# Performance work log

Measured on AMD Instinct MI355X. Metric: run time of the kernel, lower is better.

Reference implementation:

```python
import jax, jax.numpy as jnp
import numpy as np

TEMPERATURE = 10.0
N_CLASSES = 10


def _sqdist(a, b):
    # squared euclidean distances, [Na, Nb] == torch.cdist(a, b) ** 2
    an = jnp.sum(a * a, axis=1)[:, None]
    bn = jnp.sum(b * b, axis=1)[None, :]
    return jnp.maximum(an + bn - 2.0 * (a @ b.T), 0.0)


def setup_inputs() -> dict:
    key = jax.random.key(0)
    ks = jax.random.split(key, 6)
    B, N, D, H, C = 512, 4096, 512, 2048, N_CLASSES
    return {
        "x": jax.random.normal(ks[0], (B, D), dtype=jnp.float32),
        "star_features": jax.random.normal(ks[1], (N, D), dtype=jnp.float32),
        "from_features": jax.random.normal(ks[2], (N, D), dtype=jnp.float32),
        "star_label_ids": jax.random.randint(ks[3], (N,), 0, C),
        "W1": jax.random.normal(ks[4], (D, H), dtype=jnp.float32) * 0.02,
        "b1": jnp.zeros((H,), dtype=jnp.float32),
        "W2": jax.random.normal(ks[5], (H, C), dtype=jnp.float32) * 0.02,
        "b2": jnp.zeros((C,), dtype=jnp.float32),
    }


def _transport_features(x, feats_to, star_feats):
    # dists: [N_star, B]
    d = _sqdist(star_feats, x)
    d = d / jnp.mean(d, axis=0, keepdims=True)
    e = jnp.exp(-TEMPERATURE * d)                    # [N_star, B]
    w = feats_to.T @ e                               # [d_to, B]
    return (w / jnp.sum(e, axis=0, keepdims=True)).T  # [B, d_to]


def reference(x, star_features, from_features, star_label_ids, W1, b1, W2, b2):
    B = x.shape[0]
    C = N_CLASSES
    # --- exact-match lookup against dataset_star features (fused eq+all reduce) ---
    mask = jnp.all(x[:, None, :] == star_features[None, :, :], axis=2)  # [B, N_star]
    matched = jnp.any(mask, axis=1)                                      # [B]
    match_idx = jnp.argmax(mask, axis=1)                                 # [B]
    # --- transport features: matched samples take aligned dataset sample, rest use OT map ---
    xt_unmatched = _transport_features(x, from_features, star_features)  # [B, d]
    xt_matched = from_features[match_idx]                                # [B, d]
    x_transported = jnp.where(matched[:, None], xt_matched, xt_unmatched)
    # --- run the model in the transported domain (MLP classifier) ---
    h = jax.nn.relu(x_transported @ W1 + b1)
    logits = h @ W2 + b2                                                 # [B, C]
    # --- project_labels: preds and one-hot unique labels have equal dim -> cdist/argmin branch ---
    unique_labels = jnp.eye(C, dtype=logits.dtype)
    closest = jnp.argmin(_sqdist(logits, unique_labels), axis=1)
    y_proj = unique_labels[closest]                                      # [B, C] (unused by 'all_features')
    # --- transport_labels, method='all_features': feature-distance-weighted average of star labels ---
    d2 = _sqdist(from_features, x_transported)                           # [N_from, B]
    d2 = d2 / jnp.mean(d2, axis=0, keepdims=True)
    e2 = jnp.exp(-TEMPERATURE * d2)
    star_labels = jax.nn.one_hot(star_label_ids, C, dtype=x.dtype)       # [N_star, C]
    y_star = (star_labels.T @ e2 / jnp.sum(e2, axis=0, keepdims=True)).T  # [B, C]
    # single (model, dataset) pair -> sum/len is identity
    return y_star
```

## Files before the change

### kernel.cpp

```cpp
#include <hip/hip_runtime.h>

#define TEMP 10.0f
#define NS 4096
#define BB 512
#define DDIM 512
#define NCLS 10
#define LDSP 72

typedef short bf16x8 __attribute__((ext_vector_type(8)));
typedef float f32x4 __attribute__((ext_vector_type(4)));

__device__ inline short f2bf(float f) {
    unsigned u = __builtin_bit_cast(unsigned, f);
    u += 0x7FFFu + ((u >> 16) & 1u);
    return (short)(u >> 16);
}
__device__ inline float bf2f(short h) {
    unsigned u = ((unsigned)(unsigned short)h) << 16;
    return __builtin_bit_cast(float, u);
}

__global__ __launch_bounds__(256)
void prep(const float* __restrict__ x, const float* __restrict__ star,
          const float* __restrict__ from,
          short* __restrict__ Xb, short* __restrict__ Sb,
          short* __restrict__ FTb, short* __restrict__ Fb,
          float* __restrict__ xn2, float* __restrict__ sn2, float* __restrict__ fn2,
          float* __restrict__ scol, float* __restrict__ xcol, int* __restrict__ midx)
{
    int bid = blockIdx.x, t = threadIdx.x;
    if (bid < 2176) {
        const float* in; short* outb; float* n2; float* colb; int rowbase;
        if (bid < 1024)      { in = star; outb = Sb; n2 = sn2; colb = scol; rowbase = bid * 4; }
        else if (bid < 1152) { in = x;    outb = Xb; n2 = xn2; colb = xcol; rowbase = (bid - 1024) * 4; }
        else                 { in = from; outb = Fb; n2 = fn2; colb = nullptr; rowbase = (bid - 1152) * 4; }
        if (bid == 1024) { midx[t] = NS; midx[256 + t] = NS; }
        int row = rowbase + (t >> 6);
        int l = t & 63;
        const float4* p = (const float4*)(in + (size_t)row * DDIM) + l * 2;
        float4 a = p[0], b = p[1];
        float s = a.x*a.x + a.y*a.y + a.z*a.z + a.w*a.w
                + b.x*b.x + b.y*b.y + b.z*b.z + b.w*b.w;
        bf16x8 h;
        h[0]=f2bf(a.x); h[1]=f2bf(a.y); h[2]=f2bf(a.z); h[3]=f2bf(a.w);
        h[4]=f2bf(b.x); h[5]=f2bf(b.y); h[6]=f2bf(b.z); h[7]=f2bf(b.w);
        *(bf16x8*)(outb + (size_t)row * DDIM + l * 8) = h;
        #pragma unroll
        for (int off = 32; off > 0; off >>= 1) s += __shfl_down(s, off);
        if (l == 0) {
            n2[row] = s;
            if (colb) colb[row] = a.x;
        }
        return;
    }
    __shared__ short tile[64][LDSP];
    int tid2 = bid - 2176;
    int n0 = (tid2 & 63) * 64, d0 = (tid2 >> 6) * 64;
    int r = t >> 4, c4 = (t & 15) * 4;
    #pragma unroll
    for (int rr = 0; rr < 64; rr += 16) {
        float4 v = *(const float4*)(from + (size_t)(n0 + r + rr) * DDIM + d0 + c4);
        tile[r + rr][c4 + 0] = f2bf(v.x);
        tile[r + rr][c4 + 1] = f2bf(v.y);
        tile[r + rr][c4 + 2] = f2bf(v.z);
        tile[r + rr][c4 + 3] = f2bf(v.w);
    }
    __syncthreads();
    int dr = t >> 2, nco = (t & 3) * 16;
    short tmp[16];
    #pragma unroll
    for (int q = 0; q < 16; ++q) tmp[q] = tile[nco + q][dr];
    short* op = FTb + (size_t)(d0 + dr) * NS + n0 + nco;
    *(bf16x8*)op       = *(bf16x8*)tmp;
    *(bf16x8*)(op + 8) = *(bf16x8*)(tmp + 8);
}

__global__ __launch_bounds__(256)
void match16(const float* __restrict__ x, const float* __restrict__ star,
             const float* __restrict__ scol, const float* __restrict__ xcol,
             int* __restrict__ midx)
{
    __shared__ float xl[BB];
    int t = threadIdx.x;
    *(float2*)&xl[t * 2] = *(const float2*)&xcol[t * 2];
    __syncthreads();
    int n = blockIdx.x * 256 + t;
    float sv = scol[n];
    #pragma unroll 4
    for (int b4 = 0; b4 < BB; b4 += 4) {
        float4 xv = *(const float4*)&xl[b4];
        if (xv.x == sv || xv.y == sv || xv.z == sv || xv.w == sv) {
            #pragma unroll
            for (int j = 0; j < 4; ++j) {
                int b = b4 + j;
                if (xl[b] == sv) {
                    const float* xr = x + (size_t)b * DDIM;
                    const float* sr = star + (size_t)n * DDIM;
                    bool eq = true;
                    for (int k = 0; k < DDIM && eq; k += 4) {
                        float4 a = *(const float4*)(xr + k);
                        float4 c = *(const float4*)(sr + k);
                        eq = (a.x == c.x) && (a.y == c.y) &&
                             (a.z == c.z) && (a.w == c.w);
                    }
                    if (eq) atomicMin(&midx[b], n);
                }
            }
        }
    }
}

__global__ __launch_bounds__(256)
void gemm_bt(const short* __restrict__ A, const short* __restrict__ B, int K,
             int kslab, int nt, float* __restrict__ C, int ldc, size_t cstride)
{
    __shared__ short As[2][64][LDSP];
    __shared__ short Bs[2][128][LDSP];
    int t = threadIdx.x;
    int m0 = blockIdx.x * 64;
    int n0 = blockIdx.y * 128;
    int kbase = blockIdx.z * kslab;
    float* Cp = C + (size_t)blockIdx.z * cstride;
    int wid = t >> 6, lane = t & 63;
    int wr = wid >> 1, wc = wid & 1;
    int lr = lane & 15, lk = lane >> 4;

    int ar = t >> 2, ak = (t & 3) * 16;
    int br = t >> 1, bk = (t & 1) * 32;
    const short* Ag = A + (size_t)(m0 + ar) * K + kbase + ak;
    const short* Bg = B + (size_t)(n0 + br) * K + kbase + bk;

    f32x4 acc[2][4] = {};
    bf16x8 ra0 = *(const bf16x8*)Ag;
    bf16x8 ra1 = *(const bf16x8*)(Ag + 8);
    bf16x8 rb0 = *(const bf16x8*)Bg;
    bf16x8 rb1 = *(const bf16x8*)(Bg + 8);
    bf16x8 rb2 = *(const bf16x8*)(Bg + 16);
    bf16x8 rb3 = *(const bf16x8*)(Bg + 24);
    int cur = 0;
    *(bf16x8*)&As[0][ar][ak]      = ra0;
    *(bf16x8*)&As[0][ar][ak + 8]  = ra1;
    *(bf16x8*)&Bs[0][br][bk]      = rb0;
    *(bf16x8*)&Bs[0][br][bk + 8]  = rb1;
    *(bf16x8*)&Bs[0][br][bk + 16] = rb2;
    *(bf16x8*)&Bs[0][br][bk + 24] = rb3;

    for (int it = 0; it < nt; ++it) {
        __syncthreads();
        if (it + 1 < nt) {
            int ko = (it + 1) * 64;
            ra0 = *(const bf16x8*)(Ag + ko);
            ra1 = *(const bf16x8*)(Ag + ko + 8);
            rb0 = *(const bf16x8*)(Bg + ko);
            rb1 = *(const bf16x8*)(Bg + ko + 8);
            rb2 = *(const bf16x8*)(Bg + ko + 16);
            rb3 = *(const bf16x8*)(Bg + ko + 24);
        }
        #pragma unroll
        for (int ks = 0; ks < 2; ++ks) {
            int k0 = ks * 32 + lk * 8;
            bf16x8 af[2], bfr[4];
            #pragma unroll
            for (int i = 0; i < 2; ++i)
                af[i] = *(const bf16x8*)&As[cur][wr * 32 + i * 16 + lr][k0];
            #pragma unroll
            for (int j = 0; j < 4; ++j)
                bfr[j] = *(const bf16x8*)&Bs[cur][wc * 64 + j * 16 + lr][k0];
            #pragma unroll
            for (int i = 0; i < 2; ++i)
                #pragma unroll
                for (int j = 0; j < 4; ++j)
                    acc[i][j] = __builtin_amdgcn_mfma_f32_16x16x32_bf16(
                        af[i], bfr[j], acc[i][j], 0, 0, 0);
        }
        if (it + 1 < nt) {
            cur ^= 1;
            *(bf16x8*)&As[cur][ar][ak]      = ra0;
            *(bf16x8*)&As[cur][ar][ak + 8]  = ra1;
            *(bf16x8*)&Bs[cur][br][bk]      = rb0;
            *(bf16x8*)&Bs[cur][br][bk + 8]  = rb1;
            *(bf16x8*)&Bs[cur][br][bk + 16] = rb2;
            *(bf16x8*)&Bs[cur][br][bk + 24] = rb3;
        }
    }
    #pragma unroll
    for (int i = 0; i < 2; ++i) {
        #pragma unroll
        for (int r = 0; r < 4; ++r) {
            int gm = m0 + wr * 32 + i * 16 + lk * 4 + r;
            #pragma unroll
            for (int j = 0; j < 4; ++j) {
                int gn = n0 + wc * 64 + j * 16 + lr;
                Cp[(size_t)gm * ldc + gn] = acc[i][j][r];
            }
        }
    }
}

__device__ inline float block_sum(float s, float* red) {
    #pragma unroll
    for (int off = 32; off > 0; off >>= 1) s += __shfl_down(s, off);
    int wid = threadIdx.x >> 6;
    if ((threadIdx.x & 63) == 0) red[wid] = s;
    __syncthreads();
    float tot = red[0] + red[1] + red[2] + red[3];
    __syncthreads();
    return tot;
}

__global__ __launch_bounds__(256)
void exp_sq(const float* __restrict__ dTp, const float* __restrict__ an2,
            const float* __restrict__ bn2, short* __restrict__ eT,
            float* __restrict__ sumE)
{
    __shared__ float red[4];
    int b = blockIdx.x;
    int t = threadIdx.x;
    const float* p0 = dTp + (size_t)b * NS;
    const float* p1 = p0 + (size_t)BB * NS;
    float a2 = an2[b];
    float v[16];
    float s = 0.f;
    #pragma unroll
    for (int q = 0; q < 4; ++q) {
        int n = t * 16 + q * 4;
        float4 u0 = *(const float4*)(p0 + n);
        float4 u1 = *(const float4*)(p1 + n);
        float4 n2 = *(const float4*)(bn2 + n);
        float4 w;
        w.x = fmaxf(a2 + n2.x - 2.0f * (u0.x + u1.x), 0.f);
        w.y = fmaxf(a2 + n2.y - 2.0f * (u0.y + u1.y), 0.f);
        w.z = fmaxf(a2 + n2.z - 2.0f * (u0.z + u1.z), 0.f);
        w.w = fmaxf(a2 + n2.w - 2.0f * (u0.w + u1.w), 0.f);
        v[q*4+0] = w.x; v[q*4+1] = w.y; v[q*4+2] = w.z; v[q*4+3] = w.w;
        s += w.x + w.y + w.z + w.w;
    }
    float tot = block_sum(s, red);
    float scale = -TEMP * (float)NS / tot;
    float se = 0.f;
    bf16x8 h0, h1;
    #pragma unroll
    for (int e = 0; e < 16; ++e) {
        float ev = __expf(v[e] * scale);
        short hh = f2bf(ev);
        se += bf2f(hh);
        if (e < 8) h0[e] = hh; else h1[e - 8] = hh;
    }
    short* op = eT + (size_t)b * NS + t * 16;
    *(bf16x8*)op       = h0;
    *(bf16x8*)(op + 8) = h1;
    float setot = block_sum(se, red);
    if (t == 0) sumE[b] = setot;
}

__global__ __launch_bounds__(256)
void xt_fin(const float* __restrict__ wpart, const float* __restrict__ sumE,
            const int* __restrict__ midx, const float* __restrict__ fromf,
            short* __restrict__ xtb, float* __restrict__ xtn2)
{
    __shared__ float red[4];
    int b = blockIdx.x;
    int t = threadIdx.x;
    int d = t * 2;
    int mi = midx[b];
    float inv = 1.0f / sumE[b];
    float v0 = 0.f, v1 = 0.f;
    #pragma unroll
    for (int sl = 0; sl < 16; ++sl) {
        float2 p = *(const float2*)(wpart + (size_t)sl * (BB * DDIM) + (size_t)b * DDIM + d);
        v0 += p.x; v1 += p.y;
    }
    v0 *= inv; v1 *= inv;
    if (mi < NS) {
        v0 = fromf[(size_t)mi * DDIM + d];
        v1 = fromf[(size_t)mi * DDIM + d + 1];
    }
    xtb[(size_t)b * DDIM + d]     = f2bf(v0);
    xtb[(size_t)b * DDIM + d + 1] = f2bf(v1);
    float tot = block_sum(v0 * v0 + v1 * v1, red);
    if (t == 0) xtn2[b] = tot;
}

__global__ __launch_bounds__(256)
void ystar_sq(const float* __restrict__ d2p, const float* __restrict__ an2,
              const float* __restrict__ bn2, const int* __restrict__ labels,
              float* __restrict__ out)
{
    __shared__ float red[4];
    __shared__ float cred[NCLS + 1][4];
    int b = blockIdx.x;
    int t = threadIdx.x;
    const float* p0 = d2p + (size_t)b * NS;
    const float* p1 = p0 + (size_t)BB * NS;
    float a2 = an2[b];
    float v[16];
    float s = 0.f;
    #pragma unroll
    for (int q = 0; q < 4; ++q) {
        int n = t * 16 + q * 4;
        float4 u0 = *(const float4*)(p0 + n);
        float4 u1 = *(const float4*)(p1 + n);
        float4 n2 = *(const float4*)(bn2 + n);
        float4 w;
        w.x = fmaxf(a2 + n2.x - 2.0f * (u0.x + u1.x), 0.f);
        w.y = fmaxf(a2 + n2.y - 2.0f * (u0.y + u1.y), 0.f);
        w.z = fmaxf(a2 + n2.z - 2.0f * (u0.z + u1.z), 0.f);
        w.w = fmaxf(a2 + n2.w - 2.0f * (u0.w + u1.w), 0.f);
        v[q*4+0] = w.x; v[q*4+1] = w.y; v[q*4+2] = w.z; v[q*4+3] = w.w;
        s += w.x + w.y + w.z + w.w;
    }
    float tot = block_sum(s, red);
    float scale = -TEMP * (float)NS / tot;
    float accs[NCLS] = {};
    float te = 0.f;
    #pragma unroll
    for (int q = 0; q < 4; ++q) {
        int4 lb = *(const int4*)(labels + t * 16 + q * 4);
        int lbl[4] = {lb.x, lb.y, lb.z, lb.w};
        #pragma unroll
        for (int e = 0; e < 4; ++e) {
            float ev = __expf(v[q * 4 + e] * scale);
            te += ev;
            #pragma unroll
            for (int c = 0; c < NCLS; ++c) accs[c] += (lbl[e] == c) ? ev : 0.f;
        }
    }
    int wid = t >> 6, lane = t & 63;
    #pragma unroll
    for (int c = 0; c < NCLS + 1; ++c) {
        float sv = (c < NCLS) ? accs[c] : te;
        #pragma unroll
        for (int off = 32; off > 0; off >>= 1) sv += __shfl_down(sv, off);
        if (lane == 0) cred[c][wid] = sv;
    }
    __syncthreads();
    if (t < NCLS) {
        float num = cred[t][0] + cred[t][1] + cred[t][2] + cred[t][3];
        float den = cred[NCLS][0] + cred[NCLS][1] + cred[NCLS][2] + cred[NCLS][3];
        out[b * NCLS + t] = num / den;
    }
}

extern "C" void kernel_launch(void* const* d_in, const int* in_sizes, int n_in,
                              void* d_out, int out_size, void* d_ws, size_t ws_size,
                              hipStream_t stream) {
    const float* x     = (const float*)d_in[0];
    const float* star  = (const float*)d_in[1];
    const float* from  = (const float*)d_in[2];
    const int*   label = (const int*)d_in[3];
    float* out = (float*)d_out;

    float* F = (float*)d_ws;
    float* dTp   = F;
    float* wpart = F + 4194304;
    float* d2p   = F + 8388608;
    short* Sb    = (short*)(F + 12582912);
    short* FTb   = (short*)(F + 13631488);
    short* Fb    = (short*)(F + 14680064);
    short* Eb    = (short*)(F + 15728640);
    short* Xb    = (short*)(F + 16777216);
    short* XTb   = (short*)(F + 16908288);
    float* sn2   = F + 17039360;
    float* fn2   = F + 17043456;
    float* xn2   = F + 17047552;
    float* xtn2  = F + 17048064;
    float* sumE  = F + 17048576;
    float* scol  = F + 17049088;
    float* xcol  = F + 17053184;
    int*   midx  = (int*)(F + 17053696);

    prep<<<2688, 256, 0, stream>>>(x, star, from, Xb, Sb, FTb, Fb,
                                   xn2, sn2, fn2, scol, xcol, midx);
    match16<<<16, 256, 0, stream>>>(x, star, scol, xcol, midx);
    gemm_bt<<<dim3(8, 32, 2), 256, 0, stream>>>(Xb, Sb, DDIM, 256, 4, dTp, NS,
                                                (size_t)BB * NS);
    exp_sq<<<BB, 256, 0, stream>>>(dTp, xn2, sn2, Eb, sumE);
    gemm_bt<<<dim3(8, 4, 16), 256, 0, stream>>>(Eb, FTb, NS, 256, 4, wpart, DDIM,
                                                (size_t)BB * DDIM);
    xt_fin<<<BB, 256, 0, stream>>>(wpart, sumE, midx, from, XTb, xtn2);
    gemm_bt<<<dim3(8, 32, 2), 256, 0, stream>>>(XTb, Fb, DDIM, 256, 4, d2p, NS,
                                                (size_t)BB * NS);
    ystar_sq<<<BB, 256, 0, stream>>>(d2p, xtn2, fn2, label, out);
}
```

Measured before the change: 76.03 us.

## Compute distance means analytically and fuse exp epilogue into distance GEMMs

```diff
diff --git a/kernel.cpp b/kernel.cpp
--- a/kernel.cpp
+++ b/kernel.cpp
@@ -18,6 +18,46 @@
 __device__ inline float bf2f(short h) {
     unsigned u = ((unsigned)(unsigned short)h) << 16;
     return __builtin_bit_cast(float, u);
+}
+
+__device__ inline float block_sum(float s, float* red) {
+    #pragma unroll
+    for (int off = 32; off > 0; off >>= 1) s += __shfl_down(s, off);
+    int wid = threadIdx.x >> 6;
+    if ((threadIdx.x & 63) == 0) red[wid] = s;
+    __syncthreads();
+    float tot = red[0] + red[1] + red[2] + red[3];
+    __syncthreads();
+    return tot;
+}
+
+__global__ __launch_bounds__(256)
+void colmeans(const float* __restrict__ star, const float* __restrict__ from,
+              float* __restrict__ sbar, float* __restrict__ fbar,
+              float* __restrict__ sssp, float* __restrict__ fssp)
+{
+    __shared__ float csl[8][33];
+    __shared__ float red[4];
+    int bid = blockIdx.x, t = threadIdx.x;
+    const float* M; float* outm; float* outss; int ib;
+    if (bid < 16) { M = star; outm = sbar; outss = sssp; ib = bid; }
+    else          { M = from; outm = fbar; outss = fssp; ib = bid - 16; }
+    int d0 = ib * 32, rg = t >> 5, dc = t & 31;
+    float cs = 0.f, sq = 0.f;
+    #pragma unroll 4
+    for (int r = rg; r < NS; r += 8) {
+        float v = M[(size_t)r * DDIM + d0 + dc];
+        cs += v; sq += v * v;
+    }
+    csl[rg][dc] = cs;
+    float sqt = block_sum(sq, red);
+    if (t == 0) outss[ib] = sqt;
+    if (t < 32) {
+        float s = 0.f;
+        #pragma unroll
+        for (int q = 0; q < 8; ++q) s += csl[q][t];
+        outm[d0 + t] = s * (1.0f / NS);
+    }
 }
 
 __global__ __launch_bounds__(256)
@@ -76,6 +116,29 @@
 }
 
 __global__ __launch_bounds__(256)
+void scale1(const float* __restrict__ x, const float* __restrict__ sbar,
+            const float* __restrict__ sssp, const float* __restrict__ xn2,
+            float* __restrict__ escale1)
+{
+    int t = threadIdx.x;
+    int lane = t & 63, w = t >> 6;
+    int b = blockIdx.x * 4 + w;
+    const float4* xp = (const float4*)(x + (size_t)b * DDIM) + lane * 2;
+    const float4* sp = (const float4*)sbar + lane * 2;
+    float4 xa = xp[0], xb = xp[1], sa = sp[0], sb = sp[1];
+    float dot = xa.x*sa.x + xa.y*sa.y + xa.z*sa.z + xa.w*sa.w
+              + xb.x*sb.x + xb.y*sb.y + xb.z*sb.z + xb.w*sb.w;
+    float ss = (lane < 16) ? sssp[lane] : 0.f;
+    #pragma unroll
+    for (int m = 32; m > 0; m >>= 1) {
+        dot += __shfl_xor(dot, m);
+        ss  += __shfl_xor(ss, m);
+    }
+    if (lane == 0)
+        escale1[b] = -TEMP / (ss * (1.0f / NS) + xn2[b] - 2.0f * dot);
+}
+
+__global__ __launch_bounds__(256)
 void match16(const float* __restrict__ x, const float* __restrict__ star,
              const float* __restrict__ scol, const float* __restrict__ xcol,
              int* __restrict__ midx)
@@ -110,25 +173,28 @@
     }
 }
 
-__global__ __launch_bounds__(256)
-void gemm_bt(const short* __restrict__ A, const short* __restrict__ B, int K,
-             int kslab, int nt, float* __restrict__ C, int ldc, size_t cstride)
+template<int WSE>
+__global__ __launch_bounds__(256)
+void gemm_exp(const short* __restrict__ A, const short* __restrict__ B,
+              const float* __restrict__ an2, const float* __restrict__ bn2,
+              const float* __restrict__ escale, short* __restrict__ Eout,
+              float* __restrict__ sumEp)
 {
     __shared__ short As[2][64][LDSP];
     __shared__ short Bs[2][128][LDSP];
+    __shared__ float se[2][64];
+    const int K = DDIM;
     int t = threadIdx.x;
     int m0 = blockIdx.x * 64;
     int n0 = blockIdx.y * 128;
-    int kbase = blockIdx.z * kslab;
-    float* Cp = C + (size_t)blockIdx.z * cstride;
     int wid = t >> 6, lane = t & 63;
     int wr = wid >> 1, wc = wid & 1;
     int lr = lane & 15, lk = lane >> 4;
 
     int ar = t >> 2, ak = (t & 3) * 16;
     int br = t >> 1, bk = (t & 1) * 32;
-    const short* Ag = A + (size_t)(m0 + ar) * K + kbase + ak;
-    const short* Bg = B + (size_t)(n0 + br) * K + kbase + bk;
+    const short* Ag = A + (size_t)(m0 + ar) * K + ak;
+    const short* Bg = B + (size_t)(n0 + br) * K + bk;
 
     f32x4 acc[2][4] = {};
     bf16x8 ra0 = *(const bf16x8*)Ag;
@@ -145,6 +211,7 @@
     *(bf16x8*)&Bs[0][br][bk + 16] = rb2;
     *(bf16x8*)&Bs[0][br][bk + 24] = rb3;
 
+    const int nt = K / 64;
     for (int it = 0; it < nt; ++it) {
         __syncthreads();
         if (it + 1 < nt) {
@@ -183,6 +250,111 @@
             *(bf16x8*)&Bs[cur][br][bk + 24] = rb3;
         }
     }
+    float bn2v[4];
+    int gnv[4];
+    #pragma unroll
+    for (int j = 0; j < 4; ++j) { gnv[j] = n0 + wc * 64 + j * 16 + lr; bn2v[j] = bn2[gnv[j]]; }
+    #pragma unroll
+    for (int i = 0; i < 2; ++i) {
+        #pragma unroll
+        for (int r = 0; r < 4; ++r) {
+            int gm = m0 + wr * 32 + i * 16 + lk * 4 + r;
+            float a2 = an2[gm];
+            float sc = escale[gm];
+            float rs = 0.f;
+            #pragma unroll
+            for (int j = 0; j < 4; ++j) {
+                float dv = fmaxf(a2 + bn2v[j] - 2.0f * acc[i][j][r], 0.0f);
+                short hb = f2bf(__expf(dv * sc));
+                Eout[(size_t)gm * NS + gnv[j]] = hb;
+                if (WSE) rs += bf2f(hb);
+            }
+            if (WSE) {
+                #pragma unroll
+                for (int m = 1; m < 16; m <<= 1) rs += __shfl_xor(rs, m);
+                if (lr == 0) se[wc][wr * 32 + i * 16 + lk * 4 + r] = rs;
+            }
+        }
+    }
+    if (WSE) {
+        __syncthreads();
+        if (t < 64) sumEp[(size_t)(m0 + t) * 32 + blockIdx.y] = se[0][t] + se[1][t];
+    }
+}
+
+__global__ __launch_bounds__(256)
+void gemm_bt(const short* __restrict__ A, const short* __restrict__ B, int K,
+             int kslab, int nt, float* __restrict__ C, int ldc, size_t cstride)
+{
+    __shared__ short As[2][64][LDSP];
+    __shared__ short Bs[2][128][LDSP];
+    int t = threadIdx.x;
+    int m0 = blockIdx.x * 64;
+    int n0 = blockIdx.y * 128;
+    int kbase = blockIdx.z * kslab;
+    float* Cp = C + (size_t)blockIdx.z * cstride;
+    int wid = t >> 6, lane = t & 63;
+    int wr = wid >> 1, wc = wid & 1;
+    int lr = lane & 15, lk = lane >> 4;
+
+    int ar = t >> 2, ak = (t & 3) * 16;
+    int br = t >> 1, bk = (t & 1) * 32;
+    const short* Ag = A + (size_t)(m0 + ar) * K + kbase + ak;
+    const short* Bg = B + (size_t)(n0 + br) * K + kbase + bk;
+
+    f32x4 acc[2][4] = {};
+    bf16x8 ra0 = *(const bf16x8*)Ag;
+    bf16x8 ra1 = *(const bf16x8*)(Ag + 8);
+    bf16x8 rb0 = *(const bf16x8*)Bg;
+    bf16x8 rb1 = *(const bf16x8*)(Bg + 8);
+    bf16x8 rb2 = *(const bf16x8*)(Bg + 16);
+    bf16x8 rb3 = *(const bf16x8*)(Bg + 24);
+    int cur = 0;
+    *(bf16x8*)&As[0][ar][ak]      = ra0;
+    *(bf16x8*)&As[0][ar][ak + 8]  = ra1;
+    *(bf16x8*)&Bs[0][br][bk]      = rb0;
+    *(bf16x8*)&Bs[0][br][bk + 8]  = rb1;
+    *(bf16x8*)&Bs[0][br][bk + 16] = rb2;
+    *(bf16x8*)&Bs[0][br][bk + 24] = rb3;
+
+    for (int it = 0; it < nt; ++it) {
+        __syncthreads();
+        if (it + 1 < nt) {
+            int ko = (it + 1) * 64;
+            ra0 = *(const bf16x8*)(Ag + ko);
+            ra1 = *(const bf16x8*)(Ag + ko + 8);
+            rb0 = *(const bf16x8*)(Bg + ko);
+            rb1 = *(const bf16x8*)(Bg + ko + 8);
+            rb2 = *(const bf16x8*)(Bg + ko + 16);
+            rb3 = *(const bf16x8*)(Bg + ko + 24);
+        }
+        #pragma unroll
+        for (int ks = 0; ks < 2; ++ks) {
+            int k0 = ks * 32 + lk * 8;
+            bf16x8 af[2], bfr[4];
+            #pragma unroll
+            for (int i = 0; i < 2; ++i)
+                af[i] = *(const bf16x8*)&As[cur][wr * 32 + i * 16 + lr][k0];
+            #pragma unroll
+            for (int j = 0; j < 4; ++j)
+                bfr[j] = *(const bf16x8*)&Bs[cur][wc * 64 + j * 16 + lr][k0];
+            #pragma unroll
+            for (int i = 0; i < 2; ++i)
+                #pragma unroll
+                for (int j = 0; j < 4; ++j)
+                    acc[i][j] = __builtin_amdgcn_mfma_f32_16x16x32_bf16(
+                        af[i], bfr[j], acc[i][j], 0, 0, 0);
+        }
+        if (it + 1 < nt) {
+            cur ^= 1;
+            *(bf16x8*)&As[cur][ar][ak]      = ra0;
+            *(bf16x8*)&As[cur][ar][ak + 8]  = ra1;
+            *(bf16x8*)&Bs[cur][br][bk]      = rb0;
+            *(bf16x8*)&Bs[cur][br][bk + 8]  = rb1;
+            *(bf16x8*)&Bs[cur][br][bk + 16] = rb2;
+            *(bf16x8*)&Bs[cur][br][bk + 24] = rb3;
+        }
+    }
     #pragma unroll
     for (int i = 0; i < 2; ++i) {
         #pragma unroll
@@ -197,79 +369,37 @@
     }
 }
 
-__device__ inline float block_sum(float s, float* red) {
-    #pragma unroll
-    for (int off = 32; off > 0; off >>= 1) s += __shfl_down(s, off);
-    int wid = threadIdx.x >> 6;
-    if ((threadIdx.x & 63) == 0) red[wid] = s;
-    __syncthreads();
-    float tot = red[0] + red[1] + red[2] + red[3];
-    __syncthreads();
-    return tot;
-}
-
-__global__ __launch_bounds__(256)
-void exp_sq(const float* __restrict__ dTp, const float* __restrict__ an2,
-            const float* __restrict__ bn2, short* __restrict__ eT,
-            float* __restrict__ sumE)
+__global__ __launch_bounds__(256)
+void xt_fin(const float* __restrict__ wpart, const float* __restrict__ sumEp,
+            const int* __restrict__ midx, const float* __restrict__ fromf,
+            const float* __restrict__ fbar, const float* __restrict__ fssp,
+            short* __restrict__ xtb, float* __restrict__ xtn2,
+            float* __restrict__ escale2)
 {
     __shared__ float red[4];
-    int b = blockIdx.x;
-    int t = threadIdx.x;
-    const float* p0 = dTp + (size_t)b * NS;
-    const float* p1 = p0 + (size_t)BB * NS;
-    float a2 = an2[b];
-    float v[16];
-    float s = 0.f;
-    #pragma unroll
-    for (int q = 0; q < 4; ++q) {
-        int n = t * 16 + q * 4;
-        float4 u0 = *(const float4*)(p0 + n);
-        float4 u1 = *(const float4*)(p1 + n);
-        float4 n2 = *(const float4*)(bn2 + n);
-        float4 w;
-        w.x = fmaxf(a2 + n2.x - 2.0f * (u0.x + u1.x), 0.f);
-        w.y = fmaxf(a2 + n2.y - 2.0f * (u0.y + u1.y), 0.f);
-        w.z = fmaxf(a2 + n2.z - 2.0f * (u0.z + u1.z), 0.f);
-        w.w = fmaxf(a2 + n2.w - 2.0f * (u0.w + u1.w), 0.f);
-        v[q*4+0] = w.x; v[q*4+1] = w.y; v[q*4+2] = w.z; v[q*4+3] = w.w;
-        s += w.x + w.y + w.z + w.w;
-    }
-    float tot = block_sum(s, red);
-    float scale = -TEMP * (float)NS / tot;
-    float se = 0.f;
-    bf16x8 h0, h1;
-    #pragma unroll
-    for (int e = 0; e < 16; ++e) {
-        float ev = __expf(v[e] * scale);
-        short hh = f2bf(ev);
-        se += bf2f(hh);
-        if (e < 8) h0[e] = hh; else h1[e - 8] = hh;
-    }
-    short* op = eT + (size_t)b * NS + t * 16;
-    *(bf16x8*)op       = h0;
-    *(bf16x8*)(op + 8) = h1;
-    float setot = block_sum(se, red);
-    if (t == 0) sumE[b] = setot;
-}
-
-__global__ __launch_bounds__(256)
-void xt_fin(const float* __restrict__ wpart, const float* __restrict__ sumE,
-            const int* __restrict__ midx, const float* __restrict__ fromf,
-            short* __restrict__ xtb, float* __restrict__ xtn2)
-{
-    __shared__ float red[4];
+    __shared__ float bc[2];
     int b = blockIdx.x;
     int t = threadIdx.x;
     int d = t * 2;
     int mi = midx[b];
-    float inv = 1.0f / sumE[b];
+    if (t == 0) {
+        float s = 0.f;
+        #pragma unroll
+        for (int k = 0; k < 32; ++k) s += sumEp[(size_t)b * 32 + k];
+        float f = 0.f;
+        #pragma unroll
+        for (int k = 0; k < 16; ++k) f += fssp[k];
+        bc[0] = 1.0f / s;
+        bc[1] = f * (1.0f / NS);
+    }
     float v0 = 0.f, v1 = 0.f;
     #pragma unroll
     for (int sl = 0; sl < 16; ++sl) {
         float2 p = *(const float2*)(wpart + (size_t)sl * (BB * DDIM) + (size_t)b * DDIM + d);
         v0 += p.x; v1 += p.y;
     }
+    __syncthreads();
+    float inv = bc[0], fmean = bc[1];
     v0 *= inv; v1 *= inv;
     if (mi < NS) {
         v0 = fromf[(size_t)mi * DDIM + d];
@@ -277,40 +407,25 @@
     }
     xtb[(size_t)b * DDIM + d]     = f2bf(v0);
     xtb[(size_t)b * DDIM + d + 1] = f2bf(v1);
-    float tot = block_sum(v0 * v0 + v1 * v1, red);
-    if (t == 0) xtn2[b] = tot;
-}
-
-__global__ __launch_bounds__(256)
-void ystar_sq(const float* __restrict__ d2p, const float* __restrict__ an2,
-              const float* __restrict__ bn2, const int* __restrict__ labels,
-              float* __restrict__ out)
-{
-    __shared__ float red[4];
+    float nt2 = block_sum(v0 * v0 + v1 * v1, red);
+    float2 fb2 = *(const float2*)(fbar + d);
+    float fd = block_sum(v0 * fb2.x + v1 * fb2.y, red);
+    if (t == 0) {
+        xtn2[b] = nt2;
+        escale2[b] = -TEMP / (fmean + nt2 - 2.0f * fd);
+    }
+}
+
+__global__ __launch_bounds__(256)
+void ystar_fin(const short* __restrict__ e2T, const int* __restrict__ labels,
+               float* __restrict__ out)
+{
     __shared__ float cred[NCLS + 1][4];
     int b = blockIdx.x;
     int t = threadIdx.x;
-    const float* p0 = d2p + (size_t)b * NS;
-    const float* p1 = p0 + (size_t)BB * NS;
-    float a2 = an2[b];
-    float v[16];
-    float s = 0.f;
-    #pragma unroll
-    for (int q = 0; q < 4; ++q) {
-        int n = t * 16 + q * 4;
-        float4 u0 = *(const float4*)(p0 + n);
-        float4 u1 = *(const float4*)(p1 + n);
-        float4 n2 = *(const float4*)(bn2 + n);
-        float4 w;
-        w.x = fmaxf(a2 + n2.x - 2.0f * (u0.x + u1.x), 0.f);
-        w.y = fmaxf(a2 + n2.y - 2.0f * (u0.y + u1.y), 0.f);
-        w.z = fmaxf(a2 + n2.z - 2.0f * (u0.z + u1.z), 0.f);
-        w.w = fmaxf(a2 + n2.w - 2.0f * (u0.w + u1.w), 0.f);
-        v[q*4+0] = w.x; v[q*4+1] = w.y; v[q*4+2] = w.z; v[q*4+3] = w.w;
-        s += w.x + w.y + w.z + w.w;
-    }
-    float tot = block_sum(s, red);
-    float scale = -TEMP * (float)NS / tot;
+    const short* row = e2T + (size_t)b * NS + t * 16;
+    bf16x8 h0 = *(const bf16x8*)row;
+    bf16x8 h1 = *(const bf16x8*)(row + 8);
     float accs[NCLS] = {};
     float te = 0.f;
     #pragma unroll
@@ -319,7 +434,8 @@
         int lbl[4] = {lb.x, lb.y, lb.z, lb.w};
         #pragma unroll
         for (int e = 0; e < 4; ++e) {
-            float ev = __expf(v[q * 4 + e] * scale);
+            int idx = q * 4 + e;
+            float ev = bf2f(idx < 8 ? h0[idx] : h1[idx - 8]);
             te += ev;
             #pragma unroll
             for (int c = 0; c < NCLS; ++c) accs[c] += (lbl[e] == c) ? ev : 0.f;
@@ -351,34 +467,39 @@
     float* out = (float*)d_out;
 
     float* F = (float*)d_ws;
-    float* dTp   = F;
-    float* wpart = F + 4194304;
-    float* d2p   = F + 8388608;
-    short* Sb    = (short*)(F + 12582912);
-    short* FTb   = (short*)(F + 13631488);
-    short* Fb    = (short*)(F + 14680064);
-    short* Eb    = (short*)(F + 15728640);
-    short* Xb    = (short*)(F + 16777216);
-    short* XTb   = (short*)(F + 16908288);
-    float* sn2   = F + 17039360;
-    float* fn2   = F + 17043456;
-    float* xn2   = F + 17047552;
-    float* xtn2  = F + 17048064;
-    float* sumE  = F + 17048576;
-    float* scol  = F + 17049088;
-    float* xcol  = F + 17053184;
-    int*   midx  = (int*)(F + 17053696);
-
+    float* wpart = F;
+    short* Sb    = (short*)(F + 4194304);
+    short* FTb   = (short*)(F + 5242880);
+    short* Fb    = (short*)(F + 6291456);
+    short* Eb    = (short*)(F + 7340032);
+    short* E2b   = (short*)(F + 8388608);
+    short* Xb    = (short*)(F + 9437184);
+    short* XTb   = (short*)(F + 9568256);
+    float* sn2   = F + 9699328;
+    float* fn2   = F + 9703424;
+    float* xn2   = F + 9707520;
+    float* xtn2  = F + 9708032;
+    float* esc1  = F + 9708544;
+    float* esc2  = F + 9709056;
+    float* sbar  = F + 9709568;
+    float* fbar  = F + 9710080;
+    float* sssp  = F + 9710592;
+    float* fssp  = F + 9710608;
+    float* sumEp = F + 9710624;
+    float* scol  = F + 9727008;
+    float* xcol  = F + 9731104;
+    int*   midx  = (int*)(F + 9731616);
+
+    colmeans<<<32, 256, 0, stream>>>(star, from, sbar, fbar, sssp, fssp);
     prep<<<2688, 256, 0, stream>>>(x, star, from, Xb, Sb, FTb, Fb,
                                    xn2, sn2, fn2, scol, xcol, midx);
+    scale1<<<128, 256, 0, stream>>>(x, sbar, sssp, xn2, esc1);
     match16<<<16, 256, 0, stream>>>(x, star, scol, xcol, midx);
-    gemm_bt<<<dim3(8, 32, 2), 256, 0, stream>>>(Xb, Sb, DDIM, 256, 4, dTp, NS,
-                                                (size_t)BB * NS);
-    exp_sq<<<BB, 256, 0, stream>>>(dTp, xn2, sn2, Eb, sumE);
+    gemm_exp<1><<<dim3(8, 32), 256, 0, stream>>>(Xb, Sb, xn2, sn2, esc1, Eb, sumEp);
     gemm_bt<<<dim3(8, 4, 16), 256, 0, stream>>>(Eb, FTb, NS, 256, 4, wpart, DDIM,
                                                 (size_t)BB * DDIM);
-    xt_fin<<<BB, 256, 0, stream>>>(wpart, sumE, midx, from, XTb, xtn2);
-    gemm_bt<<<dim3(8, 32, 2), 256, 0, stream>>>(XTb, Fb, DDIM, 256, 4, d2p, NS,
-                                                (size_t)BB * NS);
-    ystar_sq<<<BB, 256, 0, stream>>>(d2p, xtn2, fn2, label, out);
-}
+    xt_fin<<<BB, 256, 0, stream>>>(wpart, sumEp, midx, from, fbar, fssp,
+                                   XTb, xtn2, esc2);
+    gemm_exp<0><<<dim3(8, 32), 256, 0, stream>>>(XTb, Fb, xtn2, fn2, esc2, E2b, nullptr);
+    ystar_fin<<<BB, 256, 0, stream>>>(E2b, label, out);
+}
```

Result: slower. 121.3 us (+59.6%).
